# Kernel optimization log

Hardware: AMD Instinct MI355X
Metric: run time of the kernel (lower is better)

## Reference

```python
import jax, jax.numpy as jnp
import numpy as np

B, S, D, H = 2, 2048, 1024, 16
HD = D // H  # 64
SCALE = float(np.sqrt(HD))


def setup_inputs() -> dict:
    key = jax.random.key(0)
    ks = jax.random.split(key, 11)
    def lin(kw, kb, fan_in):
        bound = 1.0 / np.sqrt(fan_in)
        W = jax.random.uniform(kw, (D, D), jnp.float32, -bound, bound)
        b = jax.random.uniform(kb, (D,), jnp.float32, -bound, bound)
        return W, b
    Wq, bq = lin(ks[0], ks[1], D)
    Wk, bk = lin(ks[2], ks[3], D)
    Wv, bv = lin(ks[4], ks[5], D)
    Wo, bo = lin(ks[6], ks[7], D)
    q = jax.random.normal(ks[8], (B, S, D), jnp.float32)
    k = jax.random.normal(ks[9], (B, S, D), jnp.float32)
    v = jax.random.normal(ks[10], (B, S, D), jnp.float32)
    mask = jnp.ones((B, 1, S, S), jnp.int32)
    return {"q": q, "k": k, "v": v, "mask": mask,
            "Wq": Wq, "bq": bq, "Wk": Wk, "bk": bk,
            "Wv": Wv, "bv": bv, "Wo": Wo, "bo": bo}


def reference(q, k, v, mask, Wq, bq, Wk, bk, Wv, bv, Wo, bo):
    # torch Linear: x @ W.T + b
    def proj(x, W, b):
        y = x @ W.T + b                      # [B,S,D]
        return y.reshape(B, -1, H, HD).transpose(0, 2, 1, 3)  # [B,H,S,HD]
    Q = proj(q, Wq, bq)
    K = proj(k, Wk, bk)
    V = proj(v, Wv, bv)
    scores = jnp.einsum('bhqd,bhkd->bhqk', Q, K) / SCALE     # [B,H,S,S]
    scores = jnp.where(mask == 0, -1e9, scores)
    attn = jax.nn.softmax(scores, axis=-1)                   # dropout in eval mode = identity
    out = jnp.einsum('bhqk,bhkd->bhqd', attn, V)             # [B,H,S,HD]
    out = out.transpose(0, 2, 1, 3).reshape(B, -1, D)        # [B,S,D]
    return out @ Wo.T + bo
```

## Files before the change

### kernel.cpp

```cpp
#include <hip/hip_runtime.h>
#include <math.h>

#define BB 2
#define SS 2048
#define DD 1024
#define HH 16
#define HDIM 64
#define KK 1024
#define MM 4096

#define QFOLD 0.18033688011112042f

typedef _Float16 f16x2 __attribute__((ext_vector_type(2)));
typedef _Float16 f16x4 __attribute__((ext_vector_type(4)));
typedef _Float16 f16x8 __attribute__((ext_vector_type(8)));
typedef float    f32x4 __attribute__((ext_vector_type(4)));
typedef float    f32x16 __attribute__((ext_vector_type(16)));
typedef unsigned uint2v __attribute__((ext_vector_type(2)));

#define GLL16(gp, lp) __builtin_amdgcn_global_load_lds(                        \
    (const __attribute__((address_space(1))) void*)(gp),                       \
    (__attribute__((address_space(3))) void*)(lp), 16, 0, 0)

static __device__ __forceinline__ float fast_exp2(float x) {
    float r;
    asm("v_exp_f32 %0, %1" : "=v"(r) : "v"(x));
    return r;
}
static __device__ __forceinline__ unsigned cvt_pk_u(float a, float b) {
    union { f16x2 h; unsigned u; } r;
    asm("v_cvt_pkrtz_f16_f32 %0, %1, %2" : "=v"(r.h) : "v"(a), "v"(b));
    return r.u;
}

__global__ __launch_bounds__(256) void prep(
    const float* __restrict__ q,  const float* __restrict__ k,
    const float* __restrict__ v,  const float* __restrict__ wq,
    const float* __restrict__ wk, const float* __restrict__ wv,
    const float* __restrict__ wo, const int* __restrict__ mask,
    _Float16* __restrict__ qh,  _Float16* __restrict__ kh,
    _Float16* __restrict__ vh,  _Float16* __restrict__ wqh,
    _Float16* __restrict__ wkh, _Float16* __restrict__ wvh,
    _Float16* __restrict__ woh, unsigned short* __restrict__ bm16)
{
    if (blockIdx.x < 16384u) {
        const unsigned u  = blockIdx.x * 256u + threadIdx.x;
        const unsigned U1 = 1u << 20;
        const unsigned U2 = 1u << 18;
        const float* src; _Float16* dst; unsigned off;
        float sc = 1.0f;
        if (u < 3u * U1) {
            const unsigned t = u >> 20; off = u & (U1 - 1u);
            src = (t == 0) ? q  : (t == 1) ? k  : v;
            dst = (t == 0) ? qh : (t == 1) ? kh : vh;
        } else {
            const unsigned r = u - 3u * U1;
            const unsigned t = r >> 18; off = r & (U2 - 1u);
            src = (t == 0) ? wq  : (t == 1) ? wk  : (t == 2) ? wv  : wo;
            dst = (t == 0) ? wqh : (t == 1) ? wkh : (t == 2) ? wvh : woh;
            if (t == 0) sc = QFOLD;
        }
        const float4 x = ((const float4*)src)[off];
        f16x4 y;
        y[0] = (_Float16)(x.x * sc); y[1] = (_Float16)(x.y * sc);
        y[2] = (_Float16)(x.z * sc); y[3] = (_Float16)(x.w * sc);
        ((f16x4*)dst)[off] = y;
    } else {
        const size_t t = (size_t)(blockIdx.x - 16384u) * 256 + threadIdx.x;
        const int4* p = (const int4*)(mask + t * 16);
        const int4 a = p[0], b = p[1], c = p[2], d = p[3];
        unsigned vv = 0;
        vv |= (a.x != 0) << 0;  vv |= (a.y != 0) << 1;
        vv |= (a.z != 0) << 2;  vv |= (a.w != 0) << 3;
        vv |= (b.x != 0) << 4;  vv |= (b.y != 0) << 5;
        vv |= (b.z != 0) << 6;  vv |= (b.w != 0) << 7;
        vv |= (c.x != 0) << 8;  vv |= (c.y != 0) << 9;
        vv |= (c.z != 0) << 10; vv |= (c.w != 0) << 11;
        vv |= (d.x != 0) << 12; vv |= (d.y != 0) << 13;
        vv |= (d.z != 0) << 14; vv |= (d.w != 0) << 15;
        bm16[t] = (unsigned short)vv;
    }
}

#define GEMM_BODY(X, W)                                                        \
    __shared__ _Float16 As[128 * 32];                                          \
    __shared__ _Float16 Bs[64 * 32];                                           \
    const int tid  = threadIdx.x;                                              \
    const int lane = tid & 63;                                                 \
    const int lr   = lane & 15;                                                \
    const int lg   = lane >> 4;                                                \
    const int wave = tid >> 6;                                                 \
    const int wr   = wave >> 1;                                                \
    const int wc   = wave & 1;                                                 \
    const int m0 = blockIdx.y << 7;                                            \
    const int n0 = blockIdx.x << 6;                                            \
    const char* Xb = (const char*)(X);                                         \
    const char* Wb = (const char*)(W);                                         \
    const int pa0 = tid * 16;                                                  \
    const int pa1 = pa0 + 4096;                                                \
    const int ra0 = pa0 >> 6, ca0 = pa0 & 63;                                  \
    const int ra1 = pa1 >> 6, ca1 = pa1 & 63;                                  \
    const int rb0 = pa0 >> 6, cb0 = pa0 & 63;                                  \
    f32x4 acc[4][2] = {};                                                      \
    for (int k0 = 0; k0 < KK; k0 += 32) {                                      \
        GLL16(Xb + ((size_t)(m0 + ra0) * KK + k0) * 2 + ca0, (char*)As + pa0); \
        GLL16(Xb + ((size_t)(m0 + ra1) * KK + k0) * 2 + ca1, (char*)As + pa1); \
        GLL16(Wb + ((size_t)(n0 + rb0) * KK + k0) * 2 + cb0, (char*)Bs + pa0); \
        __syncthreads();                                                       \
        f16x8 af[4], bf[2];                                                    \
        _Pragma("unroll")                                                      \
        for (int mi = 0; mi < 4; ++mi)                                         \
            af[mi] = *(const f16x8*)((const char*)As +                         \
                       ((wr * 64 + mi * 16 + lr) * 64 + lg * 16));             \
        _Pragma("unroll")                                                      \
        for (int ni = 0; ni < 2; ++ni)                                         \
            bf[ni] = *(const f16x8*)((const char*)Bs +                         \
                       ((wc * 32 + ni * 16 + lr) * 64 + lg * 16));             \
        _Pragma("unroll")                                                      \
        for (int mi = 0; mi < 4; ++mi)                                         \
            _Pragma("unroll")                                                  \
            for (int ni = 0; ni < 2; ++ni)                                     \
                acc[mi][ni] = __builtin_amdgcn_mfma_f32_16x16x32_f16(          \
                    af[mi], bf[ni], acc[mi][ni], 0, 0, 0);                     \
        __syncthreads();                                                       \
    }

__global__ __launch_bounds__(256) void gemm_qkv(
    const _Float16* __restrict__ qx, const _Float16* __restrict__ kx,
    const _Float16* __restrict__ vx,
    const _Float16* __restrict__ wqh, const _Float16* __restrict__ wkh,
    const _Float16* __restrict__ wvh,
    const float* __restrict__ bq, const float* __restrict__ bk,
    const float* __restrict__ bv,
    _Float16* __restrict__ Qh, _Float16* __restrict__ Kh,
    _Float16* __restrict__ Vt)
{
    const int z = blockIdx.z;
    const _Float16* X = (z == 0) ? qx : (z == 1) ? kx : vx;
    const _Float16* W = (z == 0) ? wqh : (z == 1) ? wkh : wvh;
    const float* bias = (z == 0) ? bq : (z == 1) ? bk : bv;
    const float bsc   = (z == 0) ? QFOLD : 1.0f;
    _Float16* Yh      = (z == 0) ? Qh : Kh;

    GEMM_BODY(X, W)

    #pragma unroll
    for (int ni = 0; ni < 2; ++ni) {
        const int n  = n0 + wc * 32 + ni * 16 + lr;
        const float bv_ = bias[n] * bsc;
        #pragma unroll
        for (int mi = 0; mi < 4; ++mi) {
            const int mbase = m0 + wr * 64 + mi * 16 + lg * 4;
            if (z < 2) {
                #pragma unroll
                for (int r = 0; r < 4; ++r) {
                    const int m = mbase + r;
                    const int b_ = m >> 11, s_ = m & (SS - 1);
                    const int h_ = n >> 6,  d_ = n & (HDIM - 1);
                    Yh[(((size_t)(b_ * HH + h_)) * SS + s_) * HDIM + d_] =
                        (_Float16)(acc[mi][ni][r] + bv_);
                }
            } else {
                const int b_ = mbase >> 11, s_ = mbase & (SS - 1);
                const int h_ = n >> 6,      d_ = n & (HDIM - 1);
                f16x4 tv;
                #pragma unroll
                for (int r = 0; r < 4; ++r) tv[r] = (_Float16)(acc[mi][ni][r] + bv_);
                *(f16x4*)(Vt + (((size_t)(b_ * HH + h_)) * HDIM + d_) * SS + s_) = tv;
            }
        }
    }
}

__global__ __launch_bounds__(256) void gemm_out(
    const _Float16* __restrict__ X, const _Float16* __restrict__ W,
    const float* __restrict__ bias, float* __restrict__ Y)
{
    GEMM_BODY(X, W)

    #pragma unroll
    for (int ni = 0; ni < 2; ++ni) {
        const int n  = n0 + wc * 32 + ni * 16 + lr;
        const float bv_ = bias[n];
        #pragma unroll
        for (int mi = 0; mi < 4; ++mi) {
            const int mbase = m0 + wr * 64 + mi * 16 + lg * 4;
            #pragma unroll
            for (int r = 0; r < 4; ++r)
                Y[(size_t)(mbase + r) * DD + n] = acc[mi][ni][r] + bv_;
        }
    }
}

__global__ __launch_bounds__(256) void attn_mfma9(
    const _Float16* __restrict__ Qh, const _Float16* __restrict__ Kh,
    const _Float16* __restrict__ Vt, const unsigned long long* __restrict__ bm,
    _Float16* __restrict__ AO)
{
    __shared__ _Float16 KbufS[3][4096];
    __shared__ _Float16 VbufS[3][4096];

    const int tid  = threadIdx.x;
    const int lane = tid & 63;
    const int wq   = tid >> 6;
    const int bh   = blockIdx.x;
    const int b_   = bh >> 4;
    const int h_   = bh & (HH - 1);
    const int q0   = blockIdx.y << 7;
    const int lq   = lane & 31;
    const int hi   = lane >> 5;
    const int NT   = SS / 64;

    const int qrow = q0 + wq * 32 + lq;
    const _Float16* qbase = Qh + ((size_t)bh * SS + qrow) * HDIM;
    f16x8 qf[4];
    #pragma unroll
    for (int j = 0; j < 4; ++j)
        qf[j] = *(const f16x8*)(qbase + j * 16 + hi * 8);

    const int c0 = tid, c1 = tid + 256;
    const int kr0 = c0 >> 3, krc0 = (c0 & 7) ^ (kr0 & 7);
    const int kr1 = c1 >> 3, krc1 = (c1 & 7) ^ (kr1 & 7);
    const _Float16* gK0 = Kh + ((size_t)bh * SS + kr0) * HDIM + krc0 * 8;
    const _Float16* gK1 = Kh + ((size_t)bh * SS + kr1) * HDIM + krc1 * 8;
    const _Float16* gV0 = Vt + ((size_t)bh * HDIM + kr0) * SS + krc0 * 8;
    const _Float16* gV1 = Vt + ((size_t)bh * HDIM + kr1) * SS + krc1 * 8;
    const int woff = (tid >> 6) << 10;

    f32x16 vzero;
    #pragma unroll
    for (int i = 0; i < 16; ++i) vzero[i] = 0.f;
    f32x16 oacc0 = vzero, oacc1 = vzero, lvec = vzero;

    const unsigned long long* bmrow = bm + ((size_t)b_ * SS + qrow) * (SS / 64);
    const int kxor = lq & 7;

#define STAGE(KT, BSEL) do {                                                   \
    GLL16(gK0 + (size_t)(KT) * HDIM, (char*)KbufS[BSEL] + woff);               \
    GLL16(gK1 + (size_t)(KT) * HDIM, (char*)KbufS[BSEL] + 4096 + woff);        \
    GLL16(gV0 + (KT), (char*)VbufS[BSEL] + woff);                              \
    GLL16(gV1 + (KT), (char*)VbufS[BSEL] + 4096 + woff);                       \
  } while (0)

#define QKT(S0, S1, KB) do {                                                   \
    __builtin_amdgcn_s_setprio(1);                                             \
    {   const char* kp = (KB) + lq * 128 + ((hi ^ kxor) << 4);                 \
        const f16x8 k0 = *(const f16x8*)(kp);                                  \
        const f16x8 k1 = *(const f16x8*)(kp + 4096);                           \
        S0 = __builtin_amdgcn_mfma_f32_32x32x16_f16(k0, qf[0], vzero, 0, 0, 0);\
        S1 = __builtin_amdgcn_mfma_f32_32x32x16_f16(k1, qf[0], vzero, 0, 0, 0);\
    }                                                                          \
    _Pragma("unroll")                                                          \
    for (int j = 1; j < 4; ++j) {                                              \
        const char* kp = (KB) + lq * 128 + (((2 * j + hi) ^ kxor) << 4);       \
        const f16x8 k0 = *(const f16x8*)(kp);                                  \
        const f16x8 k1 = *(const f16x8*)(kp + 4096);                           \
        S0 = __builtin_amdgcn_mfma_f32_32x32x16_f16(k0, qf[j], S0, 0, 0, 0);   \
        S1 = __builtin_amdgcn_mfma_f32_32x32x16_f16(k1, qf[j], S1, 0, 0, 0);   \
    }                                                                          \
    __builtin_amdgcn_s_setprio(0);                                             \
  } while (0)

#define SMPV(S0, S1, BMV, VB) do {                                             \
    if (~(BMV)) {                                                              \
        const unsigned long long bsh = (BMV) >> (hi * 4);                      \
        _Pragma("unroll")                                                      \
        for (int r = 0; r < 16; ++r) {                                         \
            const int crow = (r & 3) + 8 * (r >> 2);                           \
            if (!((bsh >> crow) & 1ull))        S0[r] = -1e9f;                 \
            if (!((bsh >> (32 + crow)) & 1ull)) S1[r] = -1e9f;                 \
        }                                                                      \
    }                                                                          \
    _Pragma("unroll")                                                          \
    for (int i = 0; i < 16; ++i) {                                             \
        S0[i] = fast_exp2(S0[i]);                                              \
        S1[i] = fast_exp2(S1[i]);                                              \
    }                                                                          \
    lvec += S0; lvec += S1;                                                    \
    f16x8 Bf[2][2];                                                            \
    _Pragma("unroll")                                                          \
    for (int kh = 0; kh < 2; ++kh) {                                           \
        const int b0_ = 8 * kh;                                                \
        {   unsigned u0 = cvt_pk_u(S0[b0_ + 0], S0[b0_ + 1]);                  \
            unsigned u1 = cvt_pk_u(S0[b0_ + 2], S0[b0_ + 3]);                  \
            unsigned u2 = cvt_pk_u(S0[b0_ + 4], S0[b0_ + 5]);                  \
            unsigned u3 = cvt_pk_u(S0[b0_ + 6], S0[b0_ + 7]);                  \
            const uint2v r02 = __builtin_amdgcn_permlane32_swap(u0, u2, false, false); \
            const uint2v r13 = __builtin_amdgcn_permlane32_swap(u1, u3, false, false); \
            union { unsigned w[4]; f16x8 v; } bu;                              \
            bu.w[0] = r02[0]; bu.w[1] = r13[0];                                \
            bu.w[2] = r02[1]; bu.w[3] = r13[1];                                \
            Bf[0][kh] = bu.v;                                                  \
        }                                                                      \
        {   unsigned u0 = cvt_pk_u(S1[b0_ + 0], S1[b0_ + 1]);                  \
            unsigned u1 = cvt_pk_u(S1[b0_ + 2], S1[b0_ + 3]);                  \
            unsigned u2 = cvt_pk_u(S1[b0_ + 4], S1[b0_ + 5]);                  \
            unsigned u3 = cvt_pk_u(S1[b0_ + 6], S1[b0_ + 7]);                  \
            const uint2v r02 = __builtin_amdgcn_permlane32_swap(u0, u2, false, false); \
            const uint2v r13 = __builtin_amdgcn_permlane32_swap(u1, u3, false, false); \
            union { unsigned w[4]; f16x8 v; } bu;                              \
            bu.w[0] = r02[0]; bu.w[1] = r13[0];                                \
            bu.w[2] = r02[1]; bu.w[3] = r13[1];                                \
            Bf[1][kh] = bu.v;                                                  \
        }                                                                      \
    }                                                                          \
    __builtin_amdgcn_s_setprio(1);                                             \
    _Pragma("unroll")                                                          \
    for (int kt2 = 0; kt2 < 2; ++kt2) {                                        \
        _Pragma("unroll")                                                      \
        for (int kh = 0; kh < 2; ++kh) {                                       \
            const int chunk = kt2 * 4 + kh * 2 + hi;                           \
            const int coff  = ((chunk ^ kxor) << 4);                           \
            const f16x8 v0 = *(const f16x8*)((VB) + lq * 128 + coff);          \
            const f16x8 v1 = *(const f16x8*)((VB) + (32 + lq) * 128 + coff);   \
            oacc0 = __builtin_amdgcn_mfma_f32_32x32x16_f16(v0, Bf[kt2][kh], oacc0, 0, 0, 0); \
            oacc1 = __builtin_amdgcn_mfma_f32_32x32x16_f16(v1, Bf[kt2][kh], oacc1, 0, 0, 0); \
        }                                                                      \
    }                                                                          \
    __builtin_amdgcn_s_setprio(0);                                             \
  } while (0)

    STAGE(0, 0);
    STAGE(64, 1);
    __syncthreads();

    f32x16 sA0, sA1, sB0, sB1;
    QKT(sA0, sA1, (const char*)KbufS[0]);
    unsigned long long bmvA = bmrow[0], bmvB = 0;

    int b0 = 0, b1 = 1, b2 = 2;

    for (int t = 0; t < NT; t += 2) {
        if (t + 1 < NT) bmvB = bmrow[t + 1];
        if (t + 1 < NT) QKT(sB0, sB1, (const char*)KbufS[b1]);
        if (t + 2 < NT) STAGE((t + 2) * 64, b2);
        SMPV(sA0, sA1, bmvA, (const char*)VbufS[b0]);
        __syncthreads();
        { const int tmp = b0; b0 = b1; b1 = b2; b2 = tmp; }

        if (t + 2 < NT) bmvA = bmrow[t + 2];
        if (t + 2 < NT) QKT(sA0, sA1, (const char*)KbufS[b1]);
        if (t + 3 < NT) STAGE((t + 3) * 64, b2);
        SMPV(sB0, sB1, bmvB, (const char*)VbufS[b0]);
        __syncthreads();
        { const int tmp = b0; b0 = b1; b1 = b2; b2 = tmp; }
    }
#undef STAGE
#undef QKT
#undef SMPV

    float lsum = (lvec[0] + lvec[1]) + (lvec[2] + lvec[3]);
    lsum += (lvec[4] + lvec[5]) + (lvec[6] + lvec[7]);
    lsum += (lvec[8] + lvec[9]) + (lvec[10] + lvec[11]);
    lsum += (lvec[12] + lvec[13]) + (lvec[14] + lvec[15]);
    lsum += __shfl_xor(lsum, 32);
    const float invl = 1.0f / lsum;

    _Float16* ob = AO + ((size_t)b_ * SS + qrow) * DD + h_ * HDIM + 4 * hi;
    #pragma unroll
    for (int g = 0; g < 4; ++g) {
        f16x4 r0, r1;
        #pragma unroll
        for (int tt = 0; tt < 4; ++tt) {
            r0[tt] = (_Float16)(oacc0[4 * g + tt] * invl);
            r1[tt] = (_Float16)(oacc1[4 * g + tt] * invl);
        }
        *(f16x4*)(ob + 8 * g)      = r0;
        *(f16x4*)(ob + 32 + 8 * g) = r1;
    }
}

extern "C" void kernel_launch(void* const* d_in, const int* in_sizes, int n_in,
                              void* d_out, int out_size, void* d_ws, size_t ws_size,
                              hipStream_t stream)
{
    const float* q    = (const float*)d_in[0];
    const float* k    = (const float*)d_in[1];
    const float* v    = (const float*)d_in[2];
    const int*   mask = (const int*)d_in[3];
    const float* Wq   = (const float*)d_in[4];
    const float* bq   = (const float*)d_in[5];
    const float* Wk   = (const float*)d_in[6];
    const float* bk   = (const float*)d_in[7];
    const float* Wv   = (const float*)d_in[8];
    const float* bv   = (const float*)d_in[9];
    const float* Wo   = (const float*)d_in[10];
    const float* bo   = (const float*)d_in[11];
    float* out = (float*)d_out;

    char* w = (char*)d_ws;
    _Float16* qx  = (_Float16*)(w);
    _Float16* kx  = (_Float16*)(w + 8  * 1048576);
    _Float16* vx  = (_Float16*)(w + 16 * 1048576);
    _Float16* wqh = (_Float16*)(w + 24 * 1048576);
    _Float16* wkh = (_Float16*)(w + 26 * 1048576);
    _Float16* wvh = (_Float16*)(w + 28 * 1048576);
    _Float16* woh = (_Float16*)(w + 30 * 1048576);
    _Float16* Qh  = (_Float16*)(w + 32 * 1048576);
    _Float16* Kh  = (_Float16*)(w + 40 * 1048576);
    _Float16* Vt  = (_Float16*)(w + 48 * 1048576);
    unsigned long long* bm = (unsigned long long*)(w + 56 * 1048576);
    _Float16* AO  = (_Float16*)(w);

    prep<<<18432, 256, 0, stream>>>(q, k, v, Wq, Wk, Wv, Wo, mask,
                                    qx, kx, vx, wqh, wkh, wvh, woh,
                                    (unsigned short*)bm);

    const dim3 gqkv(DD / 64, MM / 128, 3);
    gemm_qkv<<<gqkv, 256, 0, stream>>>(qx, kx, vx, wqh, wkh, wvh,
                                       bq, bk, bv, Qh, Kh, Vt);

    const dim3 gattn(BB * HH, SS / 128);
    attn_mfma9<<<gattn, 256, 0, stream>>>(Qh, Kh, Vt, bm, AO);

    const dim3 gout(DD / 64, MM / 128);
    gemm_out<<<gout, 256, 0, stream>>>(AO, woh, bo, out);
}
```

Baseline: 154.1 us.

## Split attention over key range and merge partial outputs in a combine kernel

Attention now runs with a third grid dimension of two key splits. Each block processes half of the key/value tiles and writes a normalized fp16 partial output plus the log2 of its softmax denominator. A new combine kernel weights the two partials by their denominators and writes the head-interleaved result that the output projection reads. The aim is more blocks and shorter serial loops to fill the GPU better, at the cost of an extra launch and extra global traffic for the partials. The merge is only correct if each split shares the same softmax reference, such as a fixed max.

```diff
diff --git a/kernel.cpp b/kernel.cpp
--- a/kernel.cpp
+++ b/kernel.cpp
@@ -8,6 +8,7 @@
 #define HDIM 64
 #define KK 1024
 #define MM 4096
+#define KSPLIT 2
 
 #define QFOLD 0.18033688011112042f
 
@@ -25,6 +26,11 @@
 static __device__ __forceinline__ float fast_exp2(float x) {
     float r;
     asm("v_exp_f32 %0, %1" : "=v"(r) : "v"(x));
+    return r;
+}
+static __device__ __forceinline__ float fast_log2(float x) {
+    float r;
+    asm("v_log_f32 %0, %1" : "=v"(r) : "v"(x));
     return r;
 }
 static __device__ __forceinline__ unsigned cvt_pk_u(float a, float b) {
@@ -192,10 +198,10 @@
     }
 }
 
-__global__ __launch_bounds__(256) void attn_mfma9(
+__global__ __launch_bounds__(256) void attn_mfma11(
     const _Float16* __restrict__ Qh, const _Float16* __restrict__ Kh,
     const _Float16* __restrict__ Vt, const unsigned long long* __restrict__ bm,
-    _Float16* __restrict__ AO)
+    _Float16* __restrict__ Opart, float* __restrict__ Lpart)
 {
     __shared__ _Float16 KbufS[3][4096];
     __shared__ _Float16 VbufS[3][4096];
@@ -205,11 +211,13 @@
     const int wq   = tid >> 6;
     const int bh   = blockIdx.x;
     const int b_   = bh >> 4;
-    const int h_   = bh & (HH - 1);
     const int q0   = blockIdx.y << 7;
+    const int ks   = blockIdx.z;
     const int lq   = lane & 31;
     const int hi   = lane >> 5;
-    const int NT   = SS / 64;
+    const int NT   = SS / 64 / KSPLIT;
+    const int t0   = ks * NT;
+    const int tEnd = t0 + NT;
 
     const int qrow = q0 + wq * 32 + lq;
     const _Float16* qbase = Qh + ((size_t)bh * SS + qrow) * HDIM;
@@ -320,28 +328,28 @@
     __builtin_amdgcn_s_setprio(0);                                             \
   } while (0)
 
-    STAGE(0, 0);
-    STAGE(64, 1);
+    STAGE(t0 * 64, 0);
+    STAGE((t0 + 1) * 64, 1);
     __syncthreads();
 
     f32x16 sA0, sA1, sB0, sB1;
     QKT(sA0, sA1, (const char*)KbufS[0]);
-    unsigned long long bmvA = bmrow[0], bmvB = 0;
+    unsigned long long bmvA = bmrow[t0], bmvB = 0;
 
     int b0 = 0, b1 = 1, b2 = 2;
 
-    for (int t = 0; t < NT; t += 2) {
-        if (t + 1 < NT) bmvB = bmrow[t + 1];
-        if (t + 1 < NT) QKT(sB0, sB1, (const char*)KbufS[b1]);
-        if (t + 2 < NT) STAGE((t + 2) * 64, b2);
+    for (int t = t0; t < tEnd; t += 2) {
+        if (t + 1 < tEnd) bmvB = bmrow[t + 1];
+        if (t + 1 < tEnd) QKT(sB0, sB1, (const char*)KbufS[b1]);
+        if (t + 2 < tEnd) STAGE((t + 2) * 64, b2);
         SMPV(sA0, sA1, bmvA, (const char*)VbufS[b0]);
         __syncthreads();
         { const int tmp = b0; b0 = b1; b1 = b2; b2 = tmp; }
 
-        if (t + 2 < NT) bmvA = bmrow[t + 2];
-        if (t + 2 < NT) QKT(sA0, sA1, (const char*)KbufS[b1]);
-        if (t + 3 < NT) STAGE((t + 3) * 64, b2);
-        SMPV(sB0, sB1, bmvB, (const char*)VbufS[b0]);
+        if (t + 2 < tEnd) bmvA = bmrow[t + 2];
+        if (t + 2 < tEnd) QKT(sA0, sA1, (const char*)KbufS[b1]);
+        if (t + 3 < tEnd) STAGE((t + 3) * 64, b2);
+        if (t + 1 < tEnd) SMPV(sB0, sB1, bmvB, (const char*)VbufS[b0]);
         __syncthreads();
         { const int tmp = b0; b0 = b1; b1 = b2; b2 = tmp; }
     }
@@ -356,7 +364,8 @@
     lsum += __shfl_xor(lsum, 32);
     const float invl = 1.0f / lsum;
 
-    _Float16* ob = AO + ((size_t)b_ * SS + qrow) * DD + h_ * HDIM + 4 * hi;
+    _Float16* op = Opart + (size_t)ks * (BB * HH) * SS * HDIM
+                 + ((size_t)bh * SS + qrow) * HDIM + 4 * hi;
     #pragma unroll
     for (int g = 0; g < 4; ++g) {
         f16x4 r0, r1;
@@ -365,9 +374,38 @@
             r0[tt] = (_Float16)(oacc0[4 * g + tt] * invl);
             r1[tt] = (_Float16)(oacc1[4 * g + tt] * invl);
         }
-        *(f16x4*)(ob + 8 * g)      = r0;
-        *(f16x4*)(ob + 32 + 8 * g) = r1;
-    }
+        *(f16x4*)(op + 8 * g)      = r0;
+        *(f16x4*)(op + 32 + 8 * g) = r1;
+    }
+    if (hi == 0)
+        Lpart[(size_t)ks * (BB * HH) * SS + (size_t)bh * SS + qrow] =
+            fast_log2(lsum);
+}
+
+__global__ __launch_bounds__(256) void combine(
+    const _Float16* __restrict__ Opart, const float* __restrict__ Lpart,
+    _Float16* __restrict__ AO)
+{
+    const int tid = threadIdx.x;
+    const int row = blockIdx.x * 32 + (tid >> 3);
+    const int dc  = (tid & 7) * 8;
+    const int bh = row >> 11, s = row & (SS - 1);
+    const int b_ = bh >> 4,   h_ = bh & (HH - 1);
+    const size_t PER = (size_t)(BB * HH) * SS;
+
+    const float L0 = Lpart[row], L1 = Lpart[PER + row];
+    const float Ls = fmaxf(L0, L1);
+    const float w0 = fast_exp2(L0 - Ls);
+    const float w1 = fast_exp2(L1 - Ls);
+    const float inv = 1.0f / (w0 + w1);
+
+    const f16x8 a = *(const f16x8*)(Opart + (size_t)row * HDIM + dc);
+    const f16x8 b = *(const f16x8*)(Opart + PER * HDIM + (size_t)row * HDIM + dc);
+    f16x8 r;
+    #pragma unroll
+    for (int i = 0; i < 8; ++i)
+        r[i] = (_Float16)(((float)a[i] * w0 + (float)b[i] * w1) * inv);
+    *(f16x8*)(AO + ((size_t)b_ * SS + s) * DD + h_ * HDIM + dc) = r;
 }
 
 extern "C" void kernel_launch(void* const* d_in, const int* in_sizes, int n_in,
@@ -400,7 +438,9 @@
     _Float16* Kh  = (_Float16*)(w + 40 * 1048576);
     _Float16* Vt  = (_Float16*)(w + 48 * 1048576);
     unsigned long long* bm = (unsigned long long*)(w + 56 * 1048576);
-    _Float16* AO  = (_Float16*)(w);
+    _Float16* Opart = (_Float16*)(w + 8 * 1048576);
+    float*    Lpart = (float*)(w + 24 * 1048576);
+    _Float16* AO    = (_Float16*)(w);
 
     prep<<<18432, 256, 0, stream>>>(q, k, v, Wq, Wk, Wv, Wo, mask,
                                     qx, kx, vx, wqh, wkh, wvh, woh,
@@ -410,8 +450,10 @@
     gemm_qkv<<<gqkv, 256, 0, stream>>>(qx, kx, vx, wqh, wkh, wvh,
                                        bq, bk, bv, Qh, Kh, Vt);
 
-    const dim3 gattn(BB * HH, SS / 128);
-    attn_mfma9<<<gattn, 256, 0, stream>>>(Qh, Kh, Vt, bm, AO);
+    const dim3 gattn(BB * HH, SS / 128, KSPLIT);
+    attn_mfma11<<<gattn, 256, 0, stream>>>(Qh, Kh, Vt, bm, Opart, Lpart);
+
+    combine<<<2048, 256, 0, stream>>>(Opart, Lpart, AO);
 
     const dim3 gout(DD / 64, MM / 128);
     gemm_out<<<gout, 256, 0, stream>>>(AO, woh, bo, out);
```

After: 162.3 us. 5.4% more time.
